# Kernel optimization log

Measured on AMD Instinct MI355X. Metric: run time of the kernel, lower is better.

Reference implementation:

```python
import jax, jax.numpy as jnp
import numpy as np

CROP_SIZE = (14, 14)
NUM_LEVELS = 5
CANONICAL_SIZE = 224.0
CANONICAL_LEVEL = 1.0
EPS = 1e-7  # keras.backend.epsilon()


def _map_to_level(boxes):
    # boxes: [N, 4] (x1, y1, x2, y2) in image pixels
    w = boxes[:, 2] - boxes[:, 0]
    h = boxes[:, 3] - boxes[:, 1]
    size = jnp.sqrt(w * h)
    lv = jnp.floor(CANONICAL_LEVEL + jnp.log2(size / CANONICAL_SIZE + EPS))
    return jnp.clip(lv, 0.0, NUM_LEVELS - 1.0)


def _crop_and_resize(img, boxes, crop_size):
    # TF tf.image.crop_and_resize semantics (bilinear, extrapolation_value=0).
    # img: [H, W, C]; boxes: [N, 4] normalized (y1, x1, y2, x2)
    H, W, _ = img.shape
    ch, cw = crop_size
    y1, x1, y2, x2 = boxes[:, 0], boxes[:, 1], boxes[:, 2], boxes[:, 3]
    ty = jnp.arange(ch, dtype=boxes.dtype) / (ch - 1)
    tx = jnp.arange(cw, dtype=boxes.dtype) / (cw - 1)
    ys = (y1[:, None] * (1 - ty) + y2[:, None] * ty) * (H - 1)  # [N, ch]
    xs = (x1[:, None] * (1 - tx) + x2[:, None] * tx) * (W - 1)  # [N, cw]

    def corners(c, size):
        lo = jnp.floor(c)
        frac = c - lo
        lo_i = jnp.clip(lo, 0, size - 1).astype(jnp.int32)
        hi_i = jnp.clip(lo + 1, 0, size - 1).astype(jnp.int32)
        valid = (c >= 0) & (c <= size - 1)
        return lo_i, hi_i, frac, valid

    y0, y1i, fy, vy = corners(ys, H)
    x0, x1i, fx, vx = corners(xs, W)
    # gather 4 corners: [N, ch, cw, C]
    tl = img[y0[:, :, None], x0[:, None, :]]
    tr = img[y0[:, :, None], x1i[:, None, :]]
    bl = img[y1i[:, :, None], x0[:, None, :]]
    br = img[y1i[:, :, None], x1i[:, None, :]]
    fxb = fx[:, None, :, None]
    fyb = fy[:, :, None, None]
    top = tl + (tr - tl) * fxb
    bot = bl + (br - bl) * fxb
    out = top + (bot - top) * fyb
    mask = (vy[:, :, None] & vx[:, None, :])[:, :, :, None]
    return jnp.where(mask, out, 0.0)


def _roi_align(image_shape, boxes, scores, fpn):
    img_h = image_shape[1].astype(jnp.float32)
    img_w = image_shape[2].astype(jnp.float32)
    levels = _map_to_level(boxes)
    x1b, y1b, x2b, y2b = boxes[:, 0], boxes[:, 1], boxes[:, 2], boxes[:, 3]
    out = jnp.zeros((boxes.shape[0], CROP_SIZE[0], CROP_SIZE[1], fpn[0].shape[-1]),
                    dtype=fpn[0].dtype)
    for i, f in enumerate(fpn):
        fh = jnp.float32(f.shape[0])
        fw = jnp.float32(f.shape[1])
        # exact box normalization from the keras module
        nb = jnp.stack([
            y1b / img_h * fh / (fh - 1),
            x1b / img_w * fw / (fw - 1),
            (y2b / img_h * fh - 1) / (fh - 1),
            (x2b / img_w * fw - 1) / (fw - 1)], axis=1)
        crop = _crop_and_resize(f, nb, CROP_SIZE)
        sel = (levels == i)[:, None, None, None]
        # per-box level routing (equivalent to gather -> crop -> scatter_nd)
        out = out + jnp.where(sel, crop, 0.0)
    return out[None]  # [1, N, ch, cw, C]


def setup_inputs() -> dict:
    key = jax.random.key(0)
    ks = jax.random.split(key, 10)
    N, C, IMG = 512, 256, 1024.0
    cx = jax.random.uniform(ks[0], (N,), minval=16.0, maxval=IMG - 16.0)
    cy = jax.random.uniform(ks[1], (N,), minval=16.0, maxval=IMG - 16.0)
    # log-uniform box sizes 16..512 px so all 5 FPN levels are populated
    sz = jnp.exp(jax.random.uniform(ks[2], (N,), minval=jnp.log(16.0), maxval=jnp.log(512.0)))
    ar = jnp.exp(jax.random.uniform(ks[3], (N,), minval=jnp.log(0.5), maxval=jnp.log(2.0)))
    w = sz * jnp.sqrt(ar)
    h = sz / jnp.sqrt(ar)
    x1 = jnp.clip(cx - w / 2, 0.0, IMG)
    x2 = jnp.clip(cx + w / 2, 0.0, IMG)
    y1 = jnp.clip(cy - h / 2, 0.0, IMG)
    y2 = jnp.clip(cy + h / 2, 0.0, IMG)
    boxes = jnp.stack([x1, y1, x2, y2], axis=1)[None]  # [1, N, 4]
    scores = jax.random.uniform(ks[4], (1, N), dtype=jnp.float32)
    sizes = [256, 128, 64, 32, 16]  # FPN strides 4..64 on a 1024px image
    fpn = {f"fpn{i}": jax.random.normal(ks[5 + i], (1, s, s, C), dtype=jnp.float32)
           for i, s in enumerate(sizes)}
    return {"image_shape": jnp.array([1, 1024, 1024, 3], dtype=jnp.int32),
            "boxes": boxes, "scores": scores, **fpn}


def reference(image_shape, boxes, scores, fpn0, fpn1, fpn2, fpn3, fpn4):
    b = jax.lax.stop_gradient(boxes[0])
    s = jax.lax.stop_gradient(scores[0])
    fpn = [jax.lax.stop_gradient(f[0]) for f in (fpn0, fpn1, fpn2, fpn3, fpn4)]
    return _roi_align(image_shape, b, s, fpn)
```

## Files before the change

kernel.cpp:

```cpp
#include <hip/hip_runtime.h>


#define CROP 14
#define POS (CROP * CROP)
#define C 256
#define CANON 224.0f
#define EPSF 1e-7f

__global__ __launch_bounds__(256) void roi_align_kernel(
    const int* __restrict__ image_shape,
    const float* __restrict__ boxes,
    const float* __restrict__ f0,
    const float* __restrict__ f1,
    const float* __restrict__ f2,
    const float* __restrict__ f3,
    const float* __restrict__ f4,
    float* __restrict__ out)
{
    const int blk  = blockIdx.x;
    const int box  = blk / 49;
    const int quad = blk % 49;
    const int wave = threadIdx.x >> 6;
    const int lane = threadIdx.x & 63;
    const int p    = quad * 4 + wave;
    const int py   = p / CROP;
    const int px   = p % CROP;

    const float imgh = (float)image_shape[1];
    const float imgw = (float)image_shape[2];

    const float bx1 = boxes[box * 4 + 0];
    const float by1 = boxes[box * 4 + 1];
    const float bx2 = boxes[box * 4 + 2];
    const float by2 = boxes[box * 4 + 3];

    const float w  = bx2 - bx1;
    const float h  = by2 - by1;
    const float sz = sqrtf(w * h);
    float lvf = floorf(1.0f + log2f(sz / CANON + EPSF));
    lvf = fminf(fmaxf(lvf, 0.0f), 4.0f);
    const int lv = (int)lvf;

    const int   s  = 256 >> lv;
    const float fh = (float)s;
    const float fw = (float)s;

    const float ny1 = by1 / imgh * fh / (fh - 1.0f);
    const float nx1 = bx1 / imgw * fw / (fw - 1.0f);
    const float ny2 = (by2 / imgh * fh - 1.0f) / (fh - 1.0f);
    const float nx2 = (bx2 / imgw * fw - 1.0f) / (fw - 1.0f);

    const float ty = (float)py / (float)(CROP - 1);
    const float tx = (float)px / (float)(CROP - 1);

    const float yc = (ny1 * (1.0f - ty) + ny2 * ty) * (fh - 1.0f);
    const float xc = (nx1 * (1.0f - tx) + nx2 * tx) * (fw - 1.0f);

    const float ylo = floorf(yc);
    const float fy  = yc - ylo;
    const int y0  = (int)fminf(fmaxf(ylo,        0.0f), fh - 1.0f);
    const int y1i = (int)fminf(fmaxf(ylo + 1.0f, 0.0f), fh - 1.0f);
    const bool vy = (yc >= 0.0f) && (yc <= fh - 1.0f);

    const float xlo = floorf(xc);
    const float fx  = xc - xlo;
    const int x0  = (int)fminf(fmaxf(xlo,        0.0f), fw - 1.0f);
    const int x1i = (int)fminf(fmaxf(xlo + 1.0f, 0.0f), fw - 1.0f);
    const bool vx = (xc >= 0.0f) && (xc <= fw - 1.0f);

    const float* __restrict__ f =
        (lv == 0) ? f0 : (lv == 1) ? f1 : (lv == 2) ? f2 : (lv == 3) ? f3 : f4;

    const int cbase = lane * 4;
    const size_t otl = ((size_t)y0  * s + x0 ) * C + cbase;
    const size_t otr = ((size_t)y0  * s + x1i) * C + cbase;
    const size_t obl = ((size_t)y1i * s + x0 ) * C + cbase;
    const size_t obr = ((size_t)y1i * s + x1i) * C + cbase;

    float4 rtl = *(const float4*)(f + otl);
    float4 rtr = *(const float4*)(f + otr);
    float4 rbl = *(const float4*)(f + obl);
    float4 rbr = *(const float4*)(f + obr);

    float4 o;
    if (vy && vx) {
        float top, bot;
        top = rtl.x + (rtr.x - rtl.x) * fx;
        bot = rbl.x + (rbr.x - rbl.x) * fx;
        o.x = top + (bot - top) * fy;
        top = rtl.y + (rtr.y - rtl.y) * fx;
        bot = rbl.y + (rbr.y - rbl.y) * fx;
        o.y = top + (bot - top) * fy;
        top = rtl.z + (rtr.z - rtl.z) * fx;
        bot = rbl.z + (rbr.z - rbl.z) * fx;
        o.z = top + (bot - top) * fy;
        top = rtl.w + (rtr.w - rtl.w) * fx;
        bot = rbl.w + (rbr.w - rbl.w) * fx;
        o.w = top + (bot - top) * fy;
    } else {
        o.x = 0.0f; o.y = 0.0f; o.z = 0.0f; o.w = 0.0f;
    }

    *(float4*)(out + ((size_t)box * POS + p) * C + cbase) = o;
}

extern "C" void kernel_launch(void* const* d_in, const int* in_sizes, int n_in,
                              void* d_out, int out_size, void* d_ws, size_t ws_size,
                              hipStream_t stream) {
    const int*   image_shape = (const int*)d_in[0];
    const float* boxes       = (const float*)d_in[1];
    const float* f0 = (const float*)d_in[3];
    const float* f1 = (const float*)d_in[4];
    const float* f2 = (const float*)d_in[5];
    const float* f3 = (const float*)d_in[6];
    const float* f4 = (const float*)d_in[7];
    float* out = (float*)d_out;

    const int N = in_sizes[1] / 4;

    dim3 grid(N * 49);
    dim3 block(256);
    roi_align_kernel<<<grid, block, 0, stream>>>(
        image_shape, boxes, f0, f1, f2, f3, f4, out);
}
```

Before: 61.86 us.

## Process two crop positions per wave and remap blocks across XCDs

Each wave now handles two output positions, so the per-box level and coordinate setup is shared and eight gather loads can be in flight before any interpolation. The grid shrinks from 49 to 25 blocks per box, leaving a few idle waves in the last block of each box. Block indices are also remapped so consecutive logical blocks, which belong to the same box, land on the same XCD and can share its L2 for gathered feature rows. The cost is more registers per thread and some wasted lanes at the tail of each box.

```diff
diff --git a/kernel.cpp b/kernel.cpp
--- a/kernel.cpp
+++ b/kernel.cpp
@@ -6,6 +6,7 @@
 #define C 256
 #define CANON 224.0f
 #define EPSF 1e-7f
+#define BLK_PER_BOX 25
 
 __global__ __launch_bounds__(256) void roi_align_kernel(
     const int* __restrict__ image_shape,
@@ -17,14 +18,17 @@
     const float* __restrict__ f4,
     float* __restrict__ out)
 {
-    const int blk  = blockIdx.x;
-    const int box  = blk / 49;
-    const int quad = blk % 49;
+    const int nwg = gridDim.x;
+    const int q = nwg >> 3, r = nwg & 7;
+    const int xcd = blockIdx.x & 7, slot = blockIdx.x >> 3;
+    const int blk = (xcd < r ? xcd * (q + 1) : r * (q + 1) + (xcd - r) * q) + slot;
+
+    const int box      = blk / BLK_PER_BOX;
+    const int blkInBox = blk % BLK_PER_BOX;
     const int wave = threadIdx.x >> 6;
     const int lane = threadIdx.x & 63;
-    const int p    = quad * 4 + wave;
-    const int py   = p / CROP;
-    const int px   = p % CROP;
+    const int p0 = blkInBox * 8 + wave * 2;
+    const int p1 = p0 + 1;
 
     const float imgh = (float)image_shape[1];
     const float imgw = (float)image_shape[2];
@@ -50,58 +54,84 @@
     const float ny2 = (by2 / imgh * fh - 1.0f) / (fh - 1.0f);
     const float nx2 = (bx2 / imgw * fw - 1.0f) / (fw - 1.0f);
 
-    const float ty = (float)py / (float)(CROP - 1);
-    const float tx = (float)px / (float)(CROP - 1);
-
-    const float yc = (ny1 * (1.0f - ty) + ny2 * ty) * (fh - 1.0f);
-    const float xc = (nx1 * (1.0f - tx) + nx2 * tx) * (fw - 1.0f);
-
-    const float ylo = floorf(yc);
-    const float fy  = yc - ylo;
-    const int y0  = (int)fminf(fmaxf(ylo,        0.0f), fh - 1.0f);
-    const int y1i = (int)fminf(fmaxf(ylo + 1.0f, 0.0f), fh - 1.0f);
-    const bool vy = (yc >= 0.0f) && (yc <= fh - 1.0f);
-
-    const float xlo = floorf(xc);
-    const float fx  = xc - xlo;
-    const int x0  = (int)fminf(fmaxf(xlo,        0.0f), fw - 1.0f);
-    const int x1i = (int)fminf(fmaxf(xlo + 1.0f, 0.0f), fw - 1.0f);
-    const bool vx = (xc >= 0.0f) && (xc <= fw - 1.0f);
-
     const float* __restrict__ f =
         (lv == 0) ? f0 : (lv == 1) ? f1 : (lv == 2) ? f2 : (lv == 3) ? f3 : f4;
 
     const int cbase = lane * 4;
-    const size_t otl = ((size_t)y0  * s + x0 ) * C + cbase;
-    const size_t otr = ((size_t)y0  * s + x1i) * C + cbase;
-    const size_t obl = ((size_t)y1i * s + x0 ) * C + cbase;
-    const size_t obr = ((size_t)y1i * s + x1i) * C + cbase;
 
-    float4 rtl = *(const float4*)(f + otl);
-    float4 rtr = *(const float4*)(f + otr);
-    float4 rbl = *(const float4*)(f + obl);
-    float4 rbr = *(const float4*)(f + obr);
+    float fxA, fyA, fxB, fyB;
+    bool  vA, vB;
+    size_t aTL, aTR, aBL, aBR, bTL, bTR, bBL, bBR;
 
-    float4 o;
-    if (vy && vx) {
-        float top, bot;
-        top = rtl.x + (rtr.x - rtl.x) * fx;
-        bot = rbl.x + (rbr.x - rbl.x) * fx;
-        o.x = top + (bot - top) * fy;
-        top = rtl.y + (rtr.y - rtl.y) * fx;
-        bot = rbl.y + (rbr.y - rbl.y) * fx;
-        o.y = top + (bot - top) * fy;
-        top = rtl.z + (rtr.z - rtl.z) * fx;
-        bot = rbl.z + (rbr.z - rbl.z) * fx;
-        o.z = top + (bot - top) * fy;
-        top = rtl.w + (rtr.w - rtl.w) * fx;
-        bot = rbl.w + (rbr.w - rbl.w) * fx;
-        o.w = top + (bot - top) * fy;
-    } else {
-        o.x = 0.0f; o.y = 0.0f; o.z = 0.0f; o.w = 0.0f;
+    #pragma unroll
+    for (int k = 0; k < 2; ++k) {
+        const int p  = k ? p1 : p0;
+        const int py = p / CROP;
+        const int px = p % CROP;
+        const float ty = (float)py / (float)(CROP - 1);
+        const float tx = (float)px / (float)(CROP - 1);
+        const float yc = (ny1 * (1.0f - ty) + ny2 * ty) * (fh - 1.0f);
+        const float xc = (nx1 * (1.0f - tx) + nx2 * tx) * (fw - 1.0f);
+
+        const float ylo = floorf(yc);
+        const float fy  = yc - ylo;
+        const int y0  = (int)fminf(fmaxf(ylo,        0.0f), fh - 1.0f);
+        const int y1i = (int)fminf(fmaxf(ylo + 1.0f, 0.0f), fh - 1.0f);
+        const bool vy = (yc >= 0.0f) && (yc <= fh - 1.0f);
+
+        const float xlo = floorf(xc);
+        const float fx  = xc - xlo;
+        const int x0  = (int)fminf(fmaxf(xlo,        0.0f), fw - 1.0f);
+        const int x1i = (int)fminf(fmaxf(xlo + 1.0f, 0.0f), fw - 1.0f);
+        const bool vx = (xc >= 0.0f) && (xc <= fw - 1.0f);
+
+        const size_t tl = ((size_t)y0  * s + x0 ) * C + cbase;
+        const size_t tr = ((size_t)y0  * s + x1i) * C + cbase;
+        const size_t bl = ((size_t)y1i * s + x0 ) * C + cbase;
+        const size_t br = ((size_t)y1i * s + x1i) * C + cbase;
+        if (k == 0) { fxA=fx; fyA=fy; vA=vy&&vx; aTL=tl; aTR=tr; aBL=bl; aBR=br; }
+        else        { fxB=fx; fyB=fy; vB=vy&&vx; bTL=tl; bTR=tr; bBL=bl; bBR=br; }
     }
 
-    *(float4*)(out + ((size_t)box * POS + p) * C + cbase) = o;
+    const bool doA = (p0 < POS);
+    const bool doB = (p1 < POS);
+
+    float4 rA0, rA1, rA2, rA3, rB0, rB1, rB2, rB3;
+    if (doA) {
+        rA0 = *(const float4*)(f + aTL);
+        rA1 = *(const float4*)(f + aTR);
+        rA2 = *(const float4*)(f + aBL);
+        rA3 = *(const float4*)(f + aBR);
+    }
+    if (doB) {
+        rB0 = *(const float4*)(f + bTL);
+        rB1 = *(const float4*)(f + bTR);
+        rB2 = *(const float4*)(f + bBL);
+        rB3 = *(const float4*)(f + bBR);
+    }
+
+    if (doA) {
+        float4 o;
+        if (vA) {
+            float top, bot;
+            top = rA0.x + (rA1.x - rA0.x) * fxA; bot = rA2.x + (rA3.x - rA2.x) * fxA; o.x = top + (bot - top) * fyA;
+            top = rA0.y + (rA1.y - rA0.y) * fxA; bot = rA2.y + (rA3.y - rA2.y) * fxA; o.y = top + (bot - top) * fyA;
+            top = rA0.z + (rA1.z - rA0.z) * fxA; bot = rA2.z + (rA3.z - rA2.z) * fxA; o.z = top + (bot - top) * fyA;
+            top = rA0.w + (rA1.w - rA0.w) * fxA; bot = rA2.w + (rA3.w - rA2.w) * fxA; o.w = top + (bot - top) * fyA;
+        } else { o.x = o.y = o.z = o.w = 0.0f; }
+        *(float4*)(out + ((size_t)box * POS + p0) * C + cbase) = o;
+    }
+    if (doB) {
+        float4 o;
+        if (vB) {
+            float top, bot;
+            top = rB0.x + (rB1.x - rB0.x) * fxB; bot = rB2.x + (rB3.x - rB2.x) * fxB; o.x = top + (bot - top) * fyB;
+            top = rB0.y + (rB1.y - rB0.y) * fxB; bot = rB2.y + (rB3.y - rB2.y) * fxB; o.y = top + (bot - top) * fyB;
+            top = rB0.z + (rB1.z - rB0.z) * fxB; bot = rB2.z + (rB3.z - rB2.z) * fxB; o.z = top + (bot - top) * fyB;
+            top = rB0.w + (rB1.w - rB0.w) * fxB; bot = rB2.w + (rB3.w - rB2.w) * fxB; o.w = top + (bot - top) * fyB;
+        } else { o.x = o.y = o.z = o.w = 0.0f; }
+        *(float4*)(out + ((size_t)box * POS + p1) * C + cbase) = o;
+    }
 }
 
 extern "C" void kernel_launch(void* const* d_in, const int* in_sizes, int n_in,
@@ -118,7 +148,7 @@
 
     const int N = in_sizes[1] / 4;
 
-    dim3 grid(N * 49);
+    dim3 grid(N * BLK_PER_BOX);
     dim3 block(256);
     roi_align_kernel<<<grid, block, 0, stream>>>(
         image_shape, boxes, f0, f1, f2, f3, f4, out);
```

Result: faster. 53.05 us (-14.3%).
